# Performance work log

Measured on AMD Instinct MI355X. Metric: run time of the kernel, lower is better.

The kernel has to match this reference:

```python
import jax, jax.numpy as jnp
import numpy as np
from functools import partial

B, N, C = 16, 10647, 80   # batch, total anchors (YOLOv3@416), num classes
K = 2048                  # max candidates kept per image before NMS
SCORE_THR = 0.5
IOU_THR = 0.5


def setup_inputs() -> dict:
    key = jax.random.key(0)
    # [B, N, 4+1+C]: xywh (normalized), objectness, class probs
    y_pred = jax.random.uniform(key, (B, N, 5 + C), dtype=jnp.float32)
    return {"y_pred": y_pred}


def _xywh_to_corners(b):
    x, y, w, h = b[..., 0], b[..., 1], b[..., 2], b[..., 3]
    return jnp.stack([x - w / 2, y - h / 2, x + w / 2, y + h / 2], axis=-1)


def _pairwise_iou(boxes):  # boxes [K,4] corners -> [K,K]
    x1, y1, x2, y2 = boxes[:, 0], boxes[:, 1], boxes[:, 2], boxes[:, 3]
    area = jnp.maximum(x2 - x1, 0.0) * jnp.maximum(y2 - y1, 0.0)
    ix1 = jnp.maximum(x1[:, None], x1[None, :])
    iy1 = jnp.maximum(y1[:, None], y1[None, :])
    ix2 = jnp.minimum(x2[:, None], x2[None, :])
    iy2 = jnp.minimum(y2[:, None], y2[None, :])
    inter = jnp.maximum(ix2 - ix1, 0.0) * jnp.maximum(iy2 - iy1, 0.0)
    union = area[:, None] + area[None, :] - inter
    return inter / jnp.maximum(union, 1e-9)


def _greedy_nms_keep(boxes, valid):  # boxes [K,4] sorted by score desc, valid [K] bool
    iou = _pairwise_iou(boxes)
    idxs = jnp.arange(K)

    def body(i, keep):
        suppress = keep[i] & (idxs > i) & (iou[i] > IOU_THR)
        return keep & ~suppress

    return jax.lax.fori_loop(0, K, body, valid)


def reference(y_pred):
    boxes_xywh = y_pred[..., :4]           # [B,N,4]
    obj = y_pred[..., 4]                   # [B,N]
    cls_probs = y_pred[..., 5:]            # [B,N,C]
    scores = obj * jnp.max(cls_probs, axis=-1)  # [B,N]

    # top-K candidates per image (sorted by score desc)
    scores_k, idx = jax.lax.top_k(scores, K)             # [B,K]
    boxes_k = jnp.take_along_axis(boxes_xywh, idx[:, :, None], axis=1)  # [B,K,4]
    corners = _xywh_to_corners(boxes_k)                  # [B,K,4]

    valid = scores_k > SCORE_THR                          # [B,K]
    # NMS keep mask is a non-differentiable selection
    keep = jax.vmap(_greedy_nms_keep)(
        jax.lax.stop_gradient(corners), valid)            # [B,K] bool
    keep_f = keep.astype(scores_k.dtype)

    out_boxes = corners * keep_f[:, :, None]
    out_scores = scores_k * keep_f
    return jnp.concatenate([out_boxes, out_scores[:, :, None]], axis=-1)  # [B,K,5]
```

## Files before the change

kernel.cpp:

```cpp
#include <hip/hip_runtime.h>

#define BATCH 16
#define NROW  10647
#define ROWF  85
#define NCLS  80
#define KTOP  2048
#define MPAD  16384
#define SCORE_THR 0.5f
#define IOU_THR   0.5f

typedef unsigned long long u64;
typedef unsigned int u32;

__device__ __forceinline__ u32 enc_f32(float f) {
    u32 u = __float_as_uint(f);
    return (u & 0x80000000u) ? ~u : (u | 0x80000000u);
}
__device__ __forceinline__ float dec_f32(u32 e) {
    u32 u = (e & 0x80000000u) ? (e & 0x7FFFFFFFu) : ~e;
    return __uint_as_float(u);
}
__device__ __forceinline__ float bcast(float v, int ii) {
    return __uint_as_float(__builtin_amdgcn_readlane(__float_as_uint(v), ii));
}
__device__ __forceinline__ u64 rl64(u64 v, int l) {
    u32 lo = __builtin_amdgcn_readlane((u32)(v & 0xFFFFFFFFull), l);
    u32 hi = __builtin_amdgcn_readlane((u32)(v >> 32), l);
    return ((u64)hi << 32) | (u64)lo;
}
__device__ __forceinline__ void gload_lds16(const void* g, void* lds) {
    __builtin_amdgcn_global_load_lds(
        (const __attribute__((address_space(1))) void*)g,
        (__attribute__((address_space(3))) void*)lds, 16, 0, 0);
}
__device__ __forceinline__ void bar_lds() {
    asm volatile("s_waitcnt lgkmcnt(0)" ::: "memory");
    __builtin_amdgcn_s_barrier();
    __builtin_amdgcn_sched_barrier(0);
}

template<int J>
__device__ __forceinline__ void reg_pass(u64 v[8], int tid, int k) {
    #pragma unroll
    for (int r = 0; r < 8; ++r) {
        if (!(r & J)) {
            bool desc = (((tid * 8 + r) & k) == 0);
            u64 a = v[r], b = v[r | J];
            u64 mx = a > b ? a : b, mn = a > b ? b : a;
            v[r]     = desc ? mx : mn;
            v[r | J] = desc ? mn : mx;
        }
    }
}

__device__ __forceinline__ void shfl_pass(u64 v[8], int tid, int k, int d) {
    const bool upper = (tid & d) == 0;
    const bool desc = (((tid * 8) & k) == 0);
    const bool keepmax = (desc == upper);
    #pragma unroll
    for (int r = 0; r < 8; ++r) {
        u64 pv = __shfl_xor(v[r], d);
        u64 mx = v[r] > pv ? v[r] : pv, mn = v[r] > pv ? pv : v[r];
        v[r] = keepmax ? mx : mn;
    }
}

__device__ __forceinline__ void lds_pass(u64 v[8], int tid, u64* sm, int k, int d) {
    __syncthreads();
    #pragma unroll
    for (int r = 0; r < 8; ++r) sm[r * 256 + tid] = v[r];
    __syncthreads();
    const bool upper = (tid & d) == 0;
    const bool desc = (((tid * 8) & k) == 0);
    const bool keepmax = (desc == upper);
    const int pt = tid ^ d;
    #pragma unroll
    for (int r = 0; r < 8; ++r) {
        u64 pv = sm[r * 256 + pt];
        u64 mx = v[r] > pv ? v[r] : pv, mn = v[r] > pv ? pv : v[r];
        v[r] = keepmax ? mx : mn;
    }
}

__device__ __forceinline__ void sort2048_desc(u64 v[8], int tid, u64* sm) {
    reg_pass<1>(v, tid, 2);
    reg_pass<2>(v, tid, 4); reg_pass<1>(v, tid, 4);
    for (int k = 8; k <= 2048; k <<= 1) {
        for (int j = k >> 1; j >= 8; j >>= 1) {
            int d = j >> 3;
            if (d <= 32) shfl_pass(v, tid, k, d);
            else         lds_pass(v, tid, sm, k, d);
        }
        reg_pass<4>(v, tid, k); reg_pass<2>(v, tid, k); reg_pass<1>(v, tid, k);
    }
}

__device__ __forceinline__ void cleanup2048_desc(u64 v[8], int tid, u64* sm) {
    lds_pass(v, tid, sm, 4096, 128);
    lds_pass(v, tid, sm, 4096, 64);
    for (int d = 32; d >= 1; d >>= 1) shfl_pass(v, tid, 4096, d);
    reg_pass<4>(v, tid, 4096); reg_pass<2>(v, tid, 4096); reg_pass<1>(v, tid, 4096);
}

__global__ void score_kernel(const float* __restrict__ yp, u64* __restrict__ keys) {
    __shared__ float tile[128 * ROWF];
    const int tileIdx = blockIdx.x;
    const int b = blockIdx.y;
    const int tid = threadIdx.x;
    const int batch_lim = NROW * ROWF;
    const int tile_base = tileIdx * 128 * ROWF;

    if (tile_base < batch_lim) {
        const float* src = yp + (long long)b * batch_lim + tile_base;
        int lim_e = batch_lim - tile_base;
        if (lim_e > 128 * ROWF) lim_e = 128 * ROWF;
        const int head = (4 - ((3 * b) & 3)) & 3;
        if (lim_e >= 8) {
            const int nv = (lim_e - head) >> 2;
            for (int e = tid; e < head; e += 256) tile[e] = src[e];
            const float4* s4 = (const float4*)(src + head);
            for (int q = tid; q < nv; q += 256) {
                float4 v = s4[q];
                int o = head + q * 4;
                tile[o] = v.x; tile[o + 1] = v.y; tile[o + 2] = v.z; tile[o + 3] = v.w;
            }
            for (int e = head + nv * 4 + tid; e < lim_e; e += 256) tile[e] = src[e];
        } else {
            for (int e = tid; e < lim_e; e += 256) tile[e] = src[e];
        }
    }
    __syncthreads();

    if (tid < 128) {
        int gr = tileIdx * 128 + tid;
        u64 key = 0ULL;
        if (gr < NROW) {
            const float* r = &tile[tid * ROWF];
            float obj = r[4];
            float m = r[5];
            #pragma unroll
            for (int c = 1; c < NCLS; ++c) m = fmaxf(m, r[5 + c]);
            float s = obj * m;
            key = ((u64)enc_f32(s) << 32) | (u64)(0xFFFFFFFFu - (u32)gr);
        }
        keys[(long long)b * MPAD + gr] = key;
    }
}

__global__ void chunk_sort_kernel(u64* __restrict__ keys) {
    __shared__ u64 sm[2048];
    const int b = blockIdx.y, c = blockIdx.x, tid = threadIdx.x;
    u64* base = keys + (long long)b * MPAD + c * 2048;
    u64 v[8];
    #pragma unroll
    for (int r = 0; r < 8; ++r) v[r] = base[tid * 8 + r];
    sort2048_desc(v, tid, sm);
    #pragma unroll
    for (int r = 0; r < 8; ++r) base[tid * 8 + r] = v[r];
}

__global__ void merge_all_kernel(const u64* __restrict__ keysA,
                                 const float* __restrict__ yp,
                                 float* __restrict__ sx1, float* __restrict__ sy1,
                                 float* __restrict__ sx2, float* __restrict__ sy2,
                                 float* __restrict__ sar, float* __restrict__ ssc) {
    __shared__ u64 sm[2048];
    __shared__ u64 buf[3][2048];
    const int b = blockIdx.x, tid = threadIdx.x;
    const u64* a = keysA + (long long)b * MPAD;
    u64 v[8];

    #pragma unroll
    for (int c = 0; c < 3; ++c) {
        const u64* p = a + c * 4096;
        #pragma unroll
        for (int r = 0; r < 8; ++r) {
            int e = tid * 8 + r;
            u64 va = p[e], vb = p[4095 - e];
            v[r] = va > vb ? va : vb;
        }
        cleanup2048_desc(v, tid, sm);
        #pragma unroll
        for (int r = 0; r < 8; ++r) buf[c][tid * 8 + r] = v[r];
    }
    __syncthreads();

    #pragma unroll
    for (int r = 0; r < 8; ++r) {
        int e = tid * 8 + r;
        u64 va = buf[0][e], vb = buf[1][2047 - e];
        v[r] = va > vb ? va : vb;
    }
    cleanup2048_desc(v, tid, sm);

    #pragma unroll
    for (int r = 0; r < 8; ++r) {
        int e = tid * 8 + r;
        u64 vb = buf[2][2047 - e];
        v[r] = v[r] > vb ? v[r] : vb;
    }
    cleanup2048_desc(v, tid, sm);

    #pragma unroll
    for (int r = 0; r < 8; ++r) {
        u64 key = v[r];
        float s = dec_f32((u32)(key >> 32));
        u32 idx = 0xFFFFFFFFu - (u32)(key & 0xFFFFFFFFu);
        const float* rp = yp + (long long)b * NROW * ROWF + (long long)idx * ROWF;
        float x = rp[0], y = rp[1], w = rp[2], h = rp[3];
        float hx = w * 0.5f, hy = h * 0.5f;
        float a1 = x - hx, b1 = y - hy, a2 = x + hx, b2 = y + hy;
        int o = b * KTOP + tid * 8 + r;
        sx1[o] = a1; sy1[o] = b1; sx2[o] = a2; sy2[o] = b2;
        sar[o] = fmaxf(a2 - a1, 0.f) * fmaxf(b2 - b1, 0.f);
        ssc[o] = s;
    }
}

__global__ void mask_kernel(const float* __restrict__ sx1, const float* __restrict__ sy1,
                            const float* __restrict__ sx2, const float* __restrict__ sy2,
                            const float* __restrict__ sar, u64* __restrict__ mask,
                            u64* __restrict__ diag) {
    const int b = blockIdx.y;
    const int t = blockIdx.x * 4 + (threadIdx.x >> 6);
    const int lane = threadIdx.x & 63;

    int rb = (int)((65.0f - sqrtf(4225.0f - 8.0f * (float)t)) * 0.5f);
    while (rb * (65 - rb) / 2 > t) --rb;
    while ((rb + 1) * (64 - rb) / 2 <= t) ++rb;
    const int cb = rb + t - rb * (65 - rb) / 2;

    const int oi = b * KTOP + rb * 64 + lane;
    const int oj = b * KTOP + cb * 64 + lane;
    const float rx1 = sx1[oi], ry1 = sy1[oi], rx2 = sx2[oi], ry2 = sy2[oi], ra = sar[oi];
    const float cx1 = sx1[oj], cy1 = sy1[oj], cx2 = sx2[oj], cy2 = sy2[oj], ca = sar[oj];
    const bool dg = (rb == cb);

    u64 myword = 0ULL;
    for (int ii = 0; ii < 64; ++ii) {
        float ax1 = bcast(rx1, ii), ay1 = bcast(ry1, ii);
        float ax2 = bcast(rx2, ii), ay2 = bcast(ry2, ii);
        float aa  = bcast(ra,  ii);
        float ix1 = fmaxf(ax1, cx1);
        float iy1 = fmaxf(ay1, cy1);
        float ix2 = fminf(ax2, cx2);
        float iy2 = fminf(ay2, cy2);
        float inter = fmaxf(ix2 - ix1, 0.f) * fmaxf(iy2 - iy1, 0.f);
        float uni = aa + ca - inter;
        float iou = inter / fmaxf(uni, 1e-9f);
        bool cond = (iou > IOU_THR) && (!dg || (lane > ii));
        u64 bal = __ballot(cond);
        if (lane == ii) myword = bal;
    }
    mask[(long long)(b * KTOP + rb * 64 + lane) * 32 + cb] = myword;
    if (dg) diag[(long long)b * 2048 + rb * 64 + lane] = myword;
}

__global__ void nms_out_kernel(const float* __restrict__ sx1, const float* __restrict__ sy1,
                               const float* __restrict__ sx2, const float* __restrict__ sy2,
                               const float* __restrict__ ssc,
                               const u64* __restrict__ mask,
                               const u64* __restrict__ diag, float* __restrict__ out) {
    __shared__ u64 slots[4][2048];
    __shared__ u64 pend[8][32];
    __shared__ u64 curs;
    __shared__ u64 sbits64[32];
    __shared__ u64 keepw[32];
    const int b = blockIdx.x;
    const int tid = threadIdx.x;
    const int lane = tid & 63;
    const int wave = tid >> 6;
    const u64* mb = mask + (long long)(b * KTOP) * 32;
    const char* mbc = (const char*)mb;
    const u64* dg = diag + (long long)b * 2048;

    auto issue_block = [&](int B) {
        const char* src = mbc + (size_t)B * 16384;
        char* dst = (char*)&slots[B & 3][0];
        #pragma unroll
        for (int i = 0; i < 16; ++i)
            gload_lds16(src + i * 1024 + lane * 16, dst + i * 1024);
    };

    {
        const float* sp = ssc + b * KTOP + tid * 8;
        float4 sa = *(const float4*)(sp);
        float4 sb = *(const float4*)(sp + 4);
        unsigned bits =
            (unsigned)(sa.x > SCORE_THR)       | ((unsigned)(sa.y > SCORE_THR) << 1) |
            ((unsigned)(sa.z > SCORE_THR) << 2) | ((unsigned)(sa.w > SCORE_THR) << 3) |
            ((unsigned)(sb.x > SCORE_THR) << 4) | ((unsigned)(sb.y > SCORE_THR) << 5) |
            ((unsigned)(sb.z > SCORE_THR) << 6) | ((unsigned)(sb.w > SCORE_THR) << 7);
        ((unsigned char*)sbits64)[tid] = (unsigned char)bits;
    }
    u64 dia = 0ULL;
    if (wave == 0) dia = dg[lane];
    if (wave >= 1) issue_block(wave - 1);
    __syncthreads();

    u64 myw = 0ULL;
    if (wave == 0 && lane < 32) myw = sbits64[lane];

    #pragma unroll 1
    for (int w = 0; w < 32; ++w) {
        const u64* blk = &slots[w & 3][0];

        if (wave == 0) {
            u64 dia_next = 0ULL;
            if (w < 31) dia_next = dg[(w + 1) * 64 + lane];
            u64 cur = rl64(myw, w);
            #pragma unroll
            for (int p = 0; p < 4; ++p) {
                u64 dd[16];
                #pragma unroll
                for (int i = 0; i < 16; ++i) dd[i] = rl64(dia, p * 16 + i);
                #pragma unroll
                for (int i = 0; i < 16; ++i) {
                    u64 m = ((cur >> (p * 16 + i)) & 1ULL) ? dd[i] : 0ULL;
                    cur &= ~m;
                }
            }
            if (lane == 0) curs = cur;
            dia = dia_next;
        } else {
            const int rr = wave - 1;
            if ((w % 3) == rr && w + 3 < 32) issue_block(w + 3);
            if (((w + 1) % 3) == rr)
                asm volatile("s_waitcnt vmcnt(0)" ::: "memory");
        }
        bar_lds();

        {
            u64 curv = curs;
            const int col = tid & 31;
            const int rg  = tid >> 5;
            const u64* rp = blk + (size_t)rg * 256 + col;
            u32 bits8 = (u32)(curv >> (rg * 8)) & 0xFFu;
            u64 acc = 0ULL;
            #pragma unroll
            for (int i = 0; i < 8; ++i) {
                u64 t = rp[(size_t)i * 32];
                acc |= ((bits8 >> i) & 1u) ? t : 0ULL;
            }
            pend[rg][col] = acc;
        }
        bar_lds();

        if (wave == 0 && lane < 32) {
            u64 cur = curs;
            u64 s = ((pend[0][lane] | pend[1][lane]) | (pend[2][lane] | pend[3][lane]))
                  | ((pend[4][lane] | pend[5][lane]) | (pend[6][lane] | pend[7][lane]));
            if (lane == w) myw = cur;
            else if (lane > w) myw &= ~s;
        }
    }

    if (wave == 0 && lane < 32) keepw[lane] = myw;
    __syncthreads();

    for (int t = tid; t < KTOP; t += 256) {
        int o = b * KTOP + t;
        float f = ((keepw[t >> 6] >> (t & 63)) & 1ULL) ? 1.0f : 0.0f;
        float* op = out + (long long)o * 5;
        op[0] = sx1[o] * f;
        op[1] = sy1[o] * f;
        op[2] = sx2[o] * f;
        op[3] = sy2[o] * f;
        op[4] = ssc[o] * f;
    }
}

extern "C" void kernel_launch(void* const* d_in, const int* in_sizes, int n_in,
                              void* d_out, int out_size, void* d_ws, size_t ws_size,
                              hipStream_t stream) {
    const float* yp = (const float*)d_in[0];
    float* out = (float*)d_out;
    char* ws = (char*)d_ws;

    const size_t MASK_BYTES = (size_t)BATCH * KTOP * 32 * sizeof(u64);
    const size_t SOA_BYTES  = (size_t)6 * BATCH * KTOP * sizeof(float);
    u64* keysA = (u64*)ws;
    u64* mask  = (u64*)ws;
    float* soa = (float*)(ws + MASK_BYTES);
    u64* diag  = (u64*)(ws + MASK_BYTES + SOA_BYTES);
    const int SA = BATCH * KTOP;
    float* sx1 = soa + 0 * SA;
    float* sy1 = soa + 1 * SA;
    float* sx2 = soa + 2 * SA;
    float* sy2 = soa + 3 * SA;
    float* sar = soa + 4 * SA;
    float* ssc = soa + 5 * SA;

    score_kernel<<<dim3(96, BATCH), 256, 0, stream>>>(yp, keysA);
    chunk_sort_kernel<<<dim3(6, BATCH), 256, 0, stream>>>(keysA);
    merge_all_kernel<<<BATCH, 256, 0, stream>>>(keysA, yp, sx1, sy1, sx2, sy2, sar, ssc);
    mask_kernel<<<dim3(132, BATCH), 256, 0, stream>>>(sx1, sy1, sx2, sy2, sar, mask, diag);
    nms_out_kernel<<<BATCH, 256, 0, stream>>>(sx1, sy1, sx2, sy2, ssc, mask, diag, out);
}
```

Before: 165.8 us.

## Split merge into parallel first round and widen NMS scan with register prefetch

The first merge round now runs in its own kernel across 3 blocks per image instead of serially inside one block, and the result is written to a second key buffer. The NMS output kernel moves to 1024 threads. Fifteen waves prefetch mask blocks into registers five blocks ahead, replacing the async global-to-LDS loads, and store them into a padded LDS tile. This exposes more parallelism in the merge and more memory-level parallelism in the serial NMS scan, at the cost of an extra kernel launch, a global round trip for the keys, and heavier barrier synchronisation across 16 waves.

```diff
diff --git a/kernel.cpp b/kernel.cpp
--- a/kernel.cpp
+++ b/kernel.cpp
@@ -27,11 +27,6 @@
     u32 lo = __builtin_amdgcn_readlane((u32)(v & 0xFFFFFFFFull), l);
     u32 hi = __builtin_amdgcn_readlane((u32)(v >> 32), l);
     return ((u64)hi << 32) | (u64)lo;
-}
-__device__ __forceinline__ void gload_lds16(const void* g, void* lds) {
-    __builtin_amdgcn_global_load_lds(
-        (const __attribute__((address_space(1))) void*)g,
-        (__attribute__((address_space(3))) void*)lds, 16, 0, 0);
 }
 __device__ __forceinline__ void bar_lds() {
     asm volatile("s_waitcnt lgkmcnt(0)" ::: "memory");
@@ -159,44 +154,43 @@
     for (int r = 0; r < 8; ++r) base[tid * 8 + r] = v[r];
 }
 
-__global__ void merge_all_kernel(const u64* __restrict__ keysA,
-                                 const float* __restrict__ yp,
-                                 float* __restrict__ sx1, float* __restrict__ sy1,
-                                 float* __restrict__ sx2, float* __restrict__ sy2,
-                                 float* __restrict__ sar, float* __restrict__ ssc) {
+__global__ void merge_r1_kernel(const u64* __restrict__ keysA, u64* __restrict__ keysB) {
     __shared__ u64 sm[2048];
-    __shared__ u64 buf[3][2048];
+    const int b = blockIdx.y, c = blockIdx.x, tid = threadIdx.x;
+    const u64* a = keysA + (long long)b * MPAD + c * 4096;
+    u64 v[8];
+    #pragma unroll
+    for (int r = 0; r < 8; ++r) {
+        int e = tid * 8 + r;
+        u64 va = a[e], vb = a[4095 - e];
+        v[r] = va > vb ? va : vb;
+    }
+    cleanup2048_desc(v, tid, sm);
+    u64* d = keysB + (long long)b * MPAD + c * 2048;
+    #pragma unroll
+    for (int r = 0; r < 8; ++r) d[tid * 8 + r] = v[r];
+}
+
+__global__ void merge_r23_gather_kernel(const u64* __restrict__ keysB,
+                                        const float* __restrict__ yp,
+                                        float* __restrict__ sx1, float* __restrict__ sy1,
+                                        float* __restrict__ sx2, float* __restrict__ sy2,
+                                        float* __restrict__ sar, float* __restrict__ ssc) {
+    __shared__ u64 sm[2048];
     const int b = blockIdx.x, tid = threadIdx.x;
-    const u64* a = keysA + (long long)b * MPAD;
+    const u64* a = keysB + (long long)b * MPAD;
     u64 v[8];
-
-    #pragma unroll
-    for (int c = 0; c < 3; ++c) {
-        const u64* p = a + c * 4096;
-        #pragma unroll
-        for (int r = 0; r < 8; ++r) {
-            int e = tid * 8 + r;
-            u64 va = p[e], vb = p[4095 - e];
-            v[r] = va > vb ? va : vb;
-        }
-        cleanup2048_desc(v, tid, sm);
-        #pragma unroll
-        for (int r = 0; r < 8; ++r) buf[c][tid * 8 + r] = v[r];
-    }
-    __syncthreads();
-
     #pragma unroll
     for (int r = 0; r < 8; ++r) {
         int e = tid * 8 + r;
-        u64 va = buf[0][e], vb = buf[1][2047 - e];
+        u64 va = a[e], vb = a[2048 + 2047 - e];
         v[r] = va > vb ? va : vb;
     }
     cleanup2048_desc(v, tid, sm);
-
     #pragma unroll
     for (int r = 0; r < 8; ++r) {
         int e = tid * 8 + r;
-        u64 vb = buf[2][2047 - e];
+        u64 vb = a[4096 + 2047 - e];
         v[r] = v[r] > vb ? v[r] : vb;
     }
     cleanup2048_desc(v, tid, sm);
@@ -261,8 +255,8 @@
                                const float* __restrict__ ssc,
                                const u64* __restrict__ mask,
                                const u64* __restrict__ diag, float* __restrict__ out) {
-    __shared__ u64 slots[4][2048];
-    __shared__ u64 pend[8][32];
+    __shared__ u64 blkS[64][33];
+    __shared__ u64 pend[16][32];
     __shared__ u64 curs;
     __shared__ u64 sbits64[32];
     __shared__ u64 keepw[32];
@@ -271,18 +265,18 @@
     const int lane = tid & 63;
     const int wave = tid >> 6;
     const u64* mb = mask + (long long)(b * KTOP) * 32;
-    const char* mbc = (const char*)mb;
     const u64* dg = diag + (long long)b * 2048;
 
-    auto issue_block = [&](int B) {
-        const char* src = mbc + (size_t)B * 16384;
-        char* dst = (char*)&slots[B & 3][0];
-        #pragma unroll
-        for (int i = 0; i < 16; ++i)
-            gload_lds16(src + i * 1024 + lane * 16, dst + i * 1024);
-    };
-
-    {
+    const int g = (wave - 1) / 3;
+    const int j = (wave - 1) % 3;
+    const int sbeg = j * 683;
+    const int send = (j == 2) ? 2048 : sbeg + 683;
+
+    u64 r[11];
+    #pragma unroll
+    for (int i = 0; i < 11; ++i) r[i] = 0ULL;
+
+    if (tid < 256) {
         const float* sp = ssc + b * KTOP + tid * 8;
         float4 sa = *(const float4*)(sp);
         float4 sb = *(const float4*)(sp + 4);
@@ -294,17 +288,23 @@
         ((unsigned char*)sbits64)[tid] = (unsigned char)bits;
     }
     u64 dia = 0ULL;
-    if (wave == 0) dia = dg[lane];
-    if (wave >= 1) issue_block(wave - 1);
-    __syncthreads();
+    if (wave == 0) {
+        dia = dg[lane];
+    } else {
+        const u64* src = mb + (size_t)g * 2048;
+        #pragma unroll
+        for (int i = 0; i < 11; ++i) {
+            int idx = sbeg + i * 64 + lane;
+            if (idx < send) r[i] = src[idx];
+        }
+    }
+    bar_lds();
 
     u64 myw = 0ULL;
     if (wave == 0 && lane < 32) myw = sbits64[lane];
 
     #pragma unroll 1
     for (int w = 0; w < 32; ++w) {
-        const u64* blk = &slots[w & 3][0];
-
         if (wave == 0) {
             u64 dia_next = 0ULL;
             if (w < 31) dia_next = dg[(w + 1) * 64 + lane];
@@ -322,25 +322,33 @@
             }
             if (lane == 0) curs = cur;
             dia = dia_next;
-        } else {
-            const int rr = wave - 1;
-            if ((w % 3) == rr && w + 3 < 32) issue_block(w + 3);
-            if (((w + 1) % 3) == rr)
-                asm volatile("s_waitcnt vmcnt(0)" ::: "memory");
+        } else if (w % 5 == g) {
+            #pragma unroll
+            for (int i = 0; i < 11; ++i) {
+                int idx = sbeg + i * 64 + lane;
+                if (idx < send) blkS[idx >> 5][idx & 31] = r[i];
+            }
+            if (w + 5 < 32) {
+                const u64* src = mb + (size_t)(w + 5) * 2048;
+                #pragma unroll
+                for (int i = 0; i < 11; ++i) {
+                    int idx = sbeg + i * 64 + lane;
+                    if (idx < send) r[i] = src[idx];
+                }
+            }
         }
         bar_lds();
 
-        {
+        if (tid < 512) {
             u64 curv = curs;
             const int col = tid & 31;
             const int rg  = tid >> 5;
-            const u64* rp = blk + (size_t)rg * 256 + col;
-            u32 bits8 = (u32)(curv >> (rg * 8)) & 0xFFu;
+            u32 bits4 = (u32)(curv >> (rg * 4)) & 0xFu;
             u64 acc = 0ULL;
             #pragma unroll
-            for (int i = 0; i < 8; ++i) {
-                u64 t = rp[(size_t)i * 32];
-                acc |= ((bits8 >> i) & 1u) ? t : 0ULL;
+            for (int i = 0; i < 4; ++i) {
+                u64 t = blkS[rg * 4 + i][col];
+                acc |= ((bits4 >> i) & 1u) ? t : 0ULL;
             }
             pend[rg][col] = acc;
         }
@@ -348,8 +356,10 @@
 
         if (wave == 0 && lane < 32) {
             u64 cur = curs;
-            u64 s = ((pend[0][lane] | pend[1][lane]) | (pend[2][lane] | pend[3][lane]))
-                  | ((pend[4][lane] | pend[5][lane]) | (pend[6][lane] | pend[7][lane]));
+            u64 s = (((pend[0][lane]  | pend[1][lane])  | (pend[2][lane]  | pend[3][lane])) |
+                     ((pend[4][lane]  | pend[5][lane])  | (pend[6][lane]  | pend[7][lane]))) |
+                    (((pend[8][lane]  | pend[9][lane])  | (pend[10][lane] | pend[11][lane])) |
+                     ((pend[12][lane] | pend[13][lane]) | (pend[14][lane] | pend[15][lane])));
             if (lane == w) myw = cur;
             else if (lane > w) myw &= ~s;
         }
@@ -358,7 +368,7 @@
     if (wave == 0 && lane < 32) keepw[lane] = myw;
     __syncthreads();
 
-    for (int t = tid; t < KTOP; t += 256) {
+    for (int t = tid; t < KTOP; t += 1024) {
         int o = b * KTOP + t;
         float f = ((keepw[t >> 6] >> (t & 63)) & 1ULL) ? 1.0f : 0.0f;
         float* op = out + (long long)o * 5;
@@ -377,9 +387,11 @@
     float* out = (float*)d_out;
     char* ws = (char*)d_ws;
 
+    const size_t KEYS_BYTES = (size_t)BATCH * MPAD * sizeof(u64);
     const size_t MASK_BYTES = (size_t)BATCH * KTOP * 32 * sizeof(u64);
     const size_t SOA_BYTES  = (size_t)6 * BATCH * KTOP * sizeof(float);
     u64* keysA = (u64*)ws;
+    u64* keysB = (u64*)(ws + KEYS_BYTES);
     u64* mask  = (u64*)ws;
     float* soa = (float*)(ws + MASK_BYTES);
     u64* diag  = (u64*)(ws + MASK_BYTES + SOA_BYTES);
@@ -393,7 +405,9 @@
 
     score_kernel<<<dim3(96, BATCH), 256, 0, stream>>>(yp, keysA);
     chunk_sort_kernel<<<dim3(6, BATCH), 256, 0, stream>>>(keysA);
-    merge_all_kernel<<<BATCH, 256, 0, stream>>>(keysA, yp, sx1, sy1, sx2, sy2, sar, ssc);
+    merge_r1_kernel<<<dim3(3, BATCH), 256, 0, stream>>>(keysA, keysB);
+    merge_r23_gather_kernel<<<BATCH, 256, 0, stream>>>(keysB, yp,
+                                                       sx1, sy1, sx2, sy2, sar, ssc);
     mask_kernel<<<dim3(132, BATCH), 256, 0, stream>>>(sx1, sy1, sx2, sy2, sar, mask, diag);
-    nms_out_kernel<<<BATCH, 256, 0, stream>>>(sx1, sy1, sx2, sy2, ssc, mask, diag, out);
-}
+    nms_out_kernel<<<BATCH, 1024, 0, stream>>>(sx1, sy1, sx2, sy2, ssc, mask, diag, out);
+}
```

New measurement: 214.9 us. +29.6%, slower.
